# Kernel tuning notes

Hardware: AMD Instinct MI355X
Metric: run time of the kernel (lower is better)

The kernel has to match this reference:

```python
import jax, jax.numpy as jnp
import numpy as np

HEADS = 8
DIM_HEAD = 64


def setup_inputs() -> dict:
    key = jax.random.key(0)
    k1, k2, k3 = jax.random.split(key, 3)
    b, hw, n, dim = 2, 1024, 64, 512
    x = jax.random.normal(k1, (b, hw, n, dim), dtype=jnp.float32)
    w_qkv = jax.random.normal(k2, (3 * HEADS * DIM_HEAD, dim), dtype=jnp.float32) * 0.02
    pos_bias = jax.random.normal(k3, (HEADS, n, n), dtype=jnp.float32)
    # one batch attends everywhere, one focuses on the present frame (eye mask)
    focus_present_mask = jnp.arange(b).astype(bool)
    return {"x": x, "w_qkv": w_qkv, "pos_bias": pos_bias,
            "focus_present_mask": focus_present_mask}


def reference(x, w_qkv, pos_bias, focus_present_mask):
    b, hw, n, dim = x.shape
    h, d = HEADS, DIM_HEAD
    scale = d ** -0.5

    # fused qkv projection (no bias)
    qkv = jnp.einsum('bsnc,ec->bsne', x, w_qkv)          # (b, hw, n, 3*h*d)
    q, k, v = jnp.split(qkv, 3, axis=-1)

    def to_heads(t):  # '... n (h d) -> ... h n d'
        return jnp.moveaxis(t.reshape(b, hw, n, h, d), 3, 2)

    q, k, v = map(to_heads, (q, k, v))                   # (b, hw, h, n, d)
    q = q * scale

    sim = jnp.einsum('bshid,bshjd->bshij', q, k)         # (b, hw, h, n, n)
    sim = sim + pos_bias                                 # broadcast (h, n, n)

    # focus-present mask: eye for focused batches, all-ones otherwise
    eye = jnp.eye(n, dtype=bool)
    ones = jnp.ones((n, n), dtype=bool)
    mask = jnp.where(focus_present_mask[:, None, None, None, None],
                     eye[None, None, None], ones[None, None, None])  # (b,1,1,n,n)
    neg_max = -jnp.finfo(sim.dtype).max
    sim = jnp.where(mask, sim, neg_max)

    attn = jax.nn.softmax(sim, axis=-1)                  # includes the amax shift
    out = jnp.einsum('bshij,bshjd->bshid', attn, v)      # (b, hw, h, n, d)
    out = jnp.moveaxis(out, 2, 3).reshape(b, hw, n, h * d)  # '... h n d -> ... n (h d)'
    return out
```

## Files before the change

### kernel.cpp

```cpp
#include <hip/hip_runtime.h>
#include <hip/hip_bf16.h>


typedef __attribute__((ext_vector_type(4))) float f32x4;
typedef __attribute__((ext_vector_type(8))) short s16x8;

#define DIM 512

__device__ __forceinline__ short f2bf(float f) {
    __hip_bfloat16 h = __float2bfloat16(f);
    return __builtin_bit_cast(short, h);
}
__device__ __forceinline__ f32x4 ntld4(const float* p) {
    return __builtin_nontemporal_load((const f32x4*)p);
}
__device__ __forceinline__ void ntst4(float* p, f32x4 v) {
    __builtin_nontemporal_store(v, (f32x4*)p);
}
__device__ __forceinline__ s16x8 pack8(f32x4 a, f32x4 b) {
    s16x8 v;
    v[0] = f2bf(a[0]); v[1] = f2bf(a[1]); v[2] = f2bf(a[2]); v[3] = f2bf(a[3]);
    v[4] = f2bf(b[0]); v[5] = f2bf(b[1]); v[6] = f2bf(b[2]); v[7] = f2bf(b[3]);
    return v;
}
__device__ __forceinline__ int xaddr(int row, int kb) {
    return (row << 10) + (kb ^ ((row & 7) << 4));
}
__device__ __forceinline__ int taddr(int row, int kb) {
    return (row << 7) + (kb ^ ((row & 7) << 4));
}

__global__ void conv_w(const float* __restrict__ w, unsigned short* __restrict__ wb) {
    int gid  = blockIdx.x * 256 + threadIdx.x;
    int lane = gid & 63;
    int ks   = (gid >> 6) & 15;
    int rowblk = gid >> 10;
    int row = rowblk * 16 + (lane & 15);
    int col = ks * 32 + (lane >> 4) * 8;
    const float* p = w + (size_t)row * DIM + col;
    f32x4 a = *(const f32x4*)p;
    f32x4 b = *(const f32x4*)(p + 4);
    float sc = (row < 512) ? 0.125f : 1.0f;
    a *= sc; b *= sc;
    *(s16x8*)(wb + (size_t)gid * 8) = pack8(a, b);
}

template<int WB16>
__device__ __forceinline__ s16x8 wfragL(const unsigned short* __restrict__ wb,
                                        const float* __restrict__ w,
                                        int rowblk, int ks, int lane) {
    if constexpr (WB16) {
        return *(const s16x8*)(wb + ((size_t)(rowblk * 16 + ks) * 64 + lane) * 8);
    } else {
        int row = rowblk * 16 + (lane & 15);
        int col = ks * 32 + (lane >> 4) * 8;
        const float* p = w + (size_t)row * DIM + col;
        f32x4 u0 = *(const f32x4*)p;
        f32x4 u1 = *(const f32x4*)(p + 4);
        float sc = (row < 512) ? 0.125f : 1.0f;
        u0 *= sc; u1 *= sc;
        return pack8(u0, u1);
    }
}

__device__ __forceinline__ bool decode_mask(const unsigned int* mk, int b) {
    unsigned int m0 = mk[0], m1 = mk[1];
    if (m0 <= 1u && m1 <= 1u) return ((b == 0) ? m0 : m1) != 0u;
    return ((const unsigned char*)mk)[b] != 0;
}

#define MFB(a, b, cc) __builtin_amdgcn_mfma_f32_16x16x32_bf16(a, b, cc, 0, 0, 0)

#define XF(ks)                                                               \
    s16x8 af0 = *(const s16x8*)(smem + xaddr(c,      (ks) * 64 + g * 16));   \
    s16x8 af1 = *(const s16x8*)(smem + xaddr(16 + c, (ks) * 64 + g * 16));   \
    s16x8 af2 = *(const s16x8*)(smem + xaddr(32 + c, (ks) * 64 + g * 16));   \
    s16x8 af3 = *(const s16x8*)(smem + xaddr(48 + c, (ks) * 64 + g * 16));

template<int WB16>
__global__ __launch_bounds__(1024, 4)
void attn_merged(const float* __restrict__ x,
                 const float* __restrict__ w,
                 const unsigned short* __restrict__ wb,
                 const float* __restrict__ pb,
                 const unsigned int* __restrict__ mk,
                 float* __restrict__ out)
{
    extern __shared__ char smem[];
    const int tid  = threadIdx.x;
    const int lane = tid & 63;
    const int wave = tid >> 6;
    const int g    = lane >> 4;
    const int c    = lane & 15;
    const int hp   = wave >> 1;
    const int hw2  = wave & 1;
    const int site = blockIdx.x;
    const bool focused = decode_mask(mk, site >> 10);
    const float* xblk   = x   + (size_t)site * (64 * DIM);
    float*       outblk = out + (size_t)site * (64 * DIM);
    const f32x4 zf = {0.f, 0.f, 0.f, 0.f};

    {
        const int row = tid >> 4, c16 = tid & 15;
        const float* gp = xblk + row * DIM;
        #pragma unroll
        for (int j = 0; j < 4; ++j) {
            f32x4 a = ntld4(gp + j * 128 + c16 * 8);
            f32x4 b = ntld4(gp + j * 128 + c16 * 8 + 4);
            *(s16x8*)(smem + xaddr(row, j * 256 + c16 * 16)) = pack8(a, b);
        }
    }
    __syncthreads();

    if (focused) {
        const int RB = 64 + hp * 4 + 2 * hw2;
        f32x4 va[2][4];
        #pragma unroll
        for (int i = 0; i < 2; ++i)
            #pragma unroll
            for (int j = 0; j < 4; ++j) va[i][j] = zf;
        #pragma unroll 4
        for (int ks = 0; ks < 16; ++ks) {
            s16x8 wv0 = wfragL<WB16>(wb, w, RB,     ks, lane);
            s16x8 wv1 = wfragL<WB16>(wb, w, RB + 1, ks, lane);
            XF(ks)
            va[0][0]=MFB(wv0,af0,va[0][0]); va[0][1]=MFB(wv0,af1,va[0][1]);
            va[0][2]=MFB(wv0,af2,va[0][2]); va[0][3]=MFB(wv0,af3,va[0][3]);
            va[1][0]=MFB(wv1,af0,va[1][0]); va[1][1]=MFB(wv1,af1,va[1][1]);
            va[1][2]=MFB(wv1,af2,va[1][2]); va[1][3]=MFB(wv1,af3,va[1][3]);
        }
        #pragma unroll
        for (int i = 0; i < 2; ++i)
            #pragma unroll
            for (int j = 0; j < 4; ++j)
                *(f32x4*)(outblk + (size_t)(j * 16 + c) * DIM
                          + hp * 64 + hw2 * 32 + i * 16 + g * 4) = va[i][j];
        return;
    }

    char* slotA = smem + hp * 8192;
    char* slotB = smem + 65536 + hp * 8192;
    const int RQ = hp * 4 + 2 * hw2;
    const int RK = 32 + hp * 4 + 2 * hw2;

    {
        f32x4 acc[4][2];
        #pragma unroll
        for (int t = 0; t < 4; ++t) { acc[t][0] = zf; acc[t][1] = zf; }
        #pragma unroll 4
        for (int ks = 0; ks < 16; ++ks) {
            s16x8 w0 = wfragL<WB16>(wb, w, RQ,     ks, lane);
            s16x8 w1 = wfragL<WB16>(wb, w, RQ + 1, ks, lane);
            XF(ks)
            acc[0][0]=MFB(af0,w0,acc[0][0]); acc[0][1]=MFB(af0,w1,acc[0][1]);
            acc[1][0]=MFB(af1,w0,acc[1][0]); acc[1][1]=MFB(af1,w1,acc[1][1]);
            acc[2][0]=MFB(af2,w0,acc[2][0]); acc[2][1]=MFB(af2,w1,acc[2][1]);
            acc[3][0]=MFB(af3,w0,acc[3][0]); acc[3][1]=MFB(af3,w1,acc[3][1]);
        }
        #pragma unroll
        for (int t = 0; t < 4; ++t)
            #pragma unroll
            for (int hc = 0; hc < 2; ++hc)
                #pragma unroll
                for (int rr = 0; rr < 4; ++rr) {
                    int row = t * 16 + g * 4 + rr;
                    int col = hw2 * 32 + hc * 16 + c;
                    *(short*)(slotB + (row << 7) + ((col * 2) ^ ((row & 7) << 4))) =
                        f2bf(acc[t][hc][rr]);
                }
    }

    s16x8 kc[4];
    {
        f32x4 acc[4][2];
        #pragma unroll
        for (int t = 0; t < 4; ++t) { acc[t][0] = zf; acc[t][1] = zf; }
        #pragma unroll 4
        for (int ks = 0; ks < 16; ++ks) {
            s16x8 w0 = wfragL<WB16>(wb, w, RK,     ks, lane);
            s16x8 w1 = wfragL<WB16>(wb, w, RK + 1, ks, lane);
            XF(ks)
            acc[0][0]=MFB(af0,w0,acc[0][0]); acc[0][1]=MFB(af0,w1,acc[0][1]);
            acc[1][0]=MFB(af1,w0,acc[1][0]); acc[1][1]=MFB(af1,w1,acc[1][1]);
            acc[2][0]=MFB(af2,w0,acc[2][0]); acc[2][1]=MFB(af2,w1,acc[2][1]);
            acc[3][0]=MFB(af3,w0,acc[3][0]); acc[3][1]=MFB(af3,w1,acc[3][1]);
        }
        #pragma unroll
        for (int t = 0; t < 4; ++t) kc[t] = pack8(acc[t][0], acc[t][1]);
    }

    s16x8 vc[4];
    #pragma unroll
    for (int sub = 0; sub < 2; ++sub) {
        const int RB = 64 + hp * 4 + 2 * hw2 + sub;
        f32x4 a0 = zf, a1 = zf, a2 = zf, a3 = zf;
        #pragma unroll 4
        for (int ks = 0; ks < 16; ++ks) {
            s16x8 wv = wfragL<WB16>(wb, w, RB, ks, lane);
            XF(ks)
            a0 = MFB(wv, af0, a0); a1 = MFB(wv, af1, a1);
            a2 = MFB(wv, af2, a2); a3 = MFB(wv, af3, a3);
        }
        vc[sub * 2]     = pack8(a0, a1);
        vc[sub * 2 + 1] = pack8(a2, a3);
    }

    __syncthreads();

    #pragma unroll
    for (int t = 0; t < 4; ++t)
        #pragma unroll
        for (int hc = 0; hc < 2; ++hc)
            #pragma unroll
            for (int rr = 0; rr < 4; ++rr) {
                int row = t * 16 + g * 4 + rr;
                int col = hw2 * 32 + hc * 16 + c;
                *(short*)(slotA + (row << 7) + ((col * 2) ^ ((row & 7) << 4))) =
                    kc[t][hc * 4 + rr];
            }
    __syncthreads();

    s16x8 qf[2][2];
    #pragma unroll
    for (int ks2 = 0; ks2 < 2; ++ks2)
        #pragma unroll
        for (int tr2 = 0; tr2 < 2; ++tr2)
            qf[ks2][tr2] = *(const s16x8*)(slotB +
                taddr((2 * hw2 + tr2) * 16 + c, ks2 * 64 + g * 16));
    __syncthreads();

    #pragma unroll
    for (int sub = 0; sub < 2; ++sub)
        #pragma unroll
        for (int t = 0; t < 4; ++t)
            #pragma unroll
            for (int rr = 0; rr < 4; ++rr) {
                int row = hw2 * 32 + sub * 16 + g * 4 + rr;
                int col = t * 16 + c;
                *(short*)(slotB + (row << 7) + ((col * 2) ^ ((row & 7) << 4))) =
                    vc[sub * 2 + (t >> 1)][(t & 1) * 4 + rr];
            }

    f32x4 sm[2][4];
    #pragma unroll
    for (int i = 0; i < 2; ++i)
        #pragma unroll
        for (int j = 0; j < 4; ++j) sm[i][j] = zf;
    #pragma unroll
    for (int ks2 = 0; ks2 < 2; ++ks2) {
        #pragma unroll
        for (int j = 0; j < 4; ++j) {
            s16x8 bk = *(const s16x8*)(slotA + taddr(j * 16 + c, ks2 * 64 + g * 16));
            sm[0][j] = MFB(qf[ks2][0], bk, sm[0][j]);
            sm[1][j] = MFB(qf[ks2][1], bk, sm[1][j]);
        }
    }

    const float* pbh = pb + hp * 4096;
    #pragma unroll
    for (int tr = 0; tr < 2; ++tr) {
        #pragma unroll
        for (int rr = 0; rr < 4; ++rr) {
            const int i = 32 * hw2 + tr * 16 + g * 4 + rr;
            float v0 = sm[tr][0][rr] + pbh[i * 64 +  0 + c];
            float v1 = sm[tr][1][rr] + pbh[i * 64 + 16 + c];
            float v2 = sm[tr][2][rr] + pbh[i * 64 + 32 + c];
            float v3 = sm[tr][3][rr] + pbh[i * 64 + 48 + c];
            float mx = fmaxf(fmaxf(v0, v1), fmaxf(v2, v3));
            mx = fmaxf(mx, __shfl_xor(mx, 1));
            mx = fmaxf(mx, __shfl_xor(mx, 2));
            mx = fmaxf(mx, __shfl_xor(mx, 4));
            mx = fmaxf(mx, __shfl_xor(mx, 8));
            float p0 = __expf(v0 - mx);
            float p1 = __expf(v1 - mx);
            float p2 = __expf(v2 - mx);
            float p3 = __expf(v3 - mx);
            float ssum = p0 + p1 + p2 + p3;
            ssum += __shfl_xor(ssum, 1);
            ssum += __shfl_xor(ssum, 2);
            ssum += __shfl_xor(ssum, 4);
            ssum += __shfl_xor(ssum, 8);
            float rinv = 1.0f / ssum;
            sm[tr][0][rr] = p0 * rinv; sm[tr][1][rr] = p1 * rinv;
            sm[tr][2][rr] = p2 * rinv; sm[tr][3][rr] = p3 * rinv;
        }
    }
    __syncthreads();

    #pragma unroll
    for (int tr = 0; tr < 2; ++tr)
        #pragma unroll
        for (int tc = 0; tc < 4; ++tc)
            #pragma unroll
            for (int rr = 0; rr < 4; ++rr) {
                int row = 32 * hw2 + tr * 16 + g * 4 + rr;
                int col = tc * 16 + c;
                *(short*)(slotA + (row << 7) + ((col * 2) ^ ((row & 7) << 4))) =
                    f2bf(sm[tr][tc][rr]);
            }
    __syncthreads();

    f32x4 ot[4][2];
    #pragma unroll
    for (int i = 0; i < 4; ++i) { ot[i][0] = zf; ot[i][1] = zf; }
    #pragma unroll
    for (int ks2 = 0; ks2 < 2; ++ks2) {
        s16x8 ba0 = *(const s16x8*)(slotA + taddr((2 * hw2 + 0) * 16 + c, ks2 * 64 + g * 16));
        s16x8 ba1 = *(const s16x8*)(slotA + taddr((2 * hw2 + 1) * 16 + c, ks2 * 64 + g * 16));
        #pragma unroll
        for (int i = 0; i < 4; ++i) {
            s16x8 av = *(const s16x8*)(slotB + taddr(i * 16 + c, ks2 * 64 + g * 16));
            ot[i][0] = MFB(av, ba0, ot[i][0]);
            ot[i][1] = MFB(av, ba1, ot[i][1]);
        }
    }

    #pragma unroll
    for (int i = 0; i < 4; ++i)
        #pragma unroll
        for (int j = 0; j < 2; ++j)
            *(f32x4*)(outblk + (size_t)(32 * hw2 + j * 16 + c) * DIM
                      + hp * 64 + i * 16 + g * 4) = ot[i][j];
}

extern "C" void kernel_launch(void* const* d_in, const int* in_sizes, int n_in,
                              void* d_out, int out_size, void* d_ws, size_t ws_size,
                              hipStream_t stream)
{
    const float* x  = (const float*)d_in[0];
    const float* w  = (const float*)d_in[1];
    const float* pb = (const float*)d_in[2];
    const unsigned int* mk = (const unsigned int*)d_in[3];
    float* out = (float*)d_out;

    const int LDS = 131072;
    const size_t wbytes = (size_t)1536 * 512 * sizeof(unsigned short);

    if (ws_size >= wbytes) {
        unsigned short* wbp = (unsigned short*)d_ws;
        conv_w<<<dim3(384), dim3(256), 0, stream>>>(w, wbp);
        hipFuncSetAttribute(reinterpret_cast<const void*>(&attn_merged<1>),
                            hipFuncAttributeMaxDynamicSharedMemorySize, LDS);
        attn_merged<1><<<dim3(2048), dim3(1024), LDS, stream>>>(x, w, wbp, pb, mk, out);
    } else {
        hipFuncSetAttribute(reinterpret_cast<const void*>(&attn_merged<0>),
                            hipFuncAttributeMaxDynamicSharedMemorySize, LDS);
        attn_merged<0><<<dim3(2048), dim3(1024), LDS, stream>>>(x, w, nullptr, pb, mk, out);
    }
}
```

Measured before the change: 293.3 us.

## Split each site across two half-head blocks and stage output through LDS

Each spatial site is now handled by two 512-thread blocks, each covering four of the eight heads, with 64KB of LDS instead of one 1024-thread block with 128KB. This lets more blocks be resident per CU and shortens each block's tail. The cost is that each block converts and loads the full x tile, so x global reads and bf16 conversion double. Q is now kept in registers and written to LDS together with K. Outputs are staged through a swizzled LDS tile and written with coalesced nontemporal stores, which adds extra syncs.

```diff
diff --git a/kernel.cpp b/kernel.cpp
--- a/kernel.cpp
+++ b/kernel.cpp
@@ -78,13 +78,13 @@
     s16x8 af3 = *(const s16x8*)(smem + xaddr(48 + c, (ks) * 64 + g * 16));
 
 template<int WB16>
-__global__ __launch_bounds__(1024, 4)
-void attn_merged(const float* __restrict__ x,
-                 const float* __restrict__ w,
-                 const unsigned short* __restrict__ wb,
-                 const float* __restrict__ pb,
-                 const unsigned int* __restrict__ mk,
-                 float* __restrict__ out)
+__global__ __launch_bounds__(512, 2)
+void attn_half(const float* __restrict__ x,
+               const float* __restrict__ w,
+               const unsigned short* __restrict__ wb,
+               const float* __restrict__ pb,
+               const unsigned int* __restrict__ mk,
+               float* __restrict__ out)
 {
     extern __shared__ char smem[];
     const int tid  = threadIdx.x;
@@ -92,28 +92,35 @@
     const int wave = tid >> 6;
     const int g    = lane >> 4;
     const int c    = lane & 15;
-    const int hp   = wave >> 1;
+    const int h2   = wave >> 1;
     const int hw2  = wave & 1;
-    const int site = blockIdx.x;
+    const int bid  = blockIdx.x;
+    const int site = bid >> 1;
+    const int half = bid & 1;
+    const int gh   = half * 4 + h2;
     const bool focused = decode_mask(mk, site >> 10);
     const float* xblk   = x   + (size_t)site * (64 * DIM);
     float*       outblk = out + (size_t)site * (64 * DIM);
     const f32x4 zf = {0.f, 0.f, 0.f, 0.f};
 
     {
-        const int row = tid >> 4, c16 = tid & 15;
-        const float* gp = xblk + row * DIM;
-        #pragma unroll
-        for (int j = 0; j < 4; ++j) {
-            f32x4 a = ntld4(gp + j * 128 + c16 * 8);
-            f32x4 b = ntld4(gp + j * 128 + c16 * 8 + 4);
-            *(s16x8*)(smem + xaddr(row, j * 256 + c16 * 16)) = pack8(a, b);
+        const int row16 = tid >> 4, c16 = tid & 15;
+        #pragma unroll
+        for (int rr2 = 0; rr2 < 2; ++rr2) {
+            const int row = row16 + rr2 * 32;
+            const float* gp = xblk + row * DIM;
+            #pragma unroll
+            for (int j = 0; j < 4; ++j) {
+                f32x4 a = ntld4(gp + j * 128 + c16 * 8);
+                f32x4 b = ntld4(gp + j * 128 + c16 * 8 + 4);
+                *(s16x8*)(smem + xaddr(row, j * 256 + c16 * 16)) = pack8(a, b);
+            }
         }
     }
     __syncthreads();
 
     if (focused) {
-        const int RB = 64 + hp * 4 + 2 * hw2;
+        const int RB = 64 + gh * 4 + 2 * hw2;
         f32x4 va[2][4];
         #pragma unroll
         for (int i = 0; i < 2; ++i)
@@ -129,20 +136,30 @@
             va[1][0]=MFB(wv1,af0,va[1][0]); va[1][1]=MFB(wv1,af1,va[1][1]);
             va[1][2]=MFB(wv1,af2,va[1][2]); va[1][3]=MFB(wv1,af3,va[1][3]);
         }
-        #pragma unroll
-        for (int i = 0; i < 2; ++i)
-            #pragma unroll
-            for (int j = 0; j < 4; ++j)
-                *(f32x4*)(outblk + (size_t)(j * 16 + c) * DIM
-                          + hp * 64 + hw2 * 32 + i * 16 + g * 4) = va[i][j];
+        __syncthreads();
+        #pragma unroll
+        for (int sub = 0; sub < 2; ++sub)
+            #pragma unroll
+            for (int tt = 0; tt < 4; ++tt) {
+                int rl   = tt * 16 + c;
+                int colb = h2 * 256 + hw2 * 128 + sub * 64 + g * 16;
+                *(f32x4*)(smem + rl * 1024 + (colb ^ ((rl & 7) << 4))) = va[sub][tt];
+            }
+        __syncthreads();
+        #pragma unroll
+        for (int i = 0; i < 8; ++i) {
+            int lin = i * 8192 + tid * 16;
+            int rl = lin >> 10, off = lin & 1023;
+            f32x4 v = *(const f32x4*)(smem + rl * 1024 + (off ^ ((rl & 7) << 4)));
+            ntst4((float*)((char*)outblk + rl * 2048 + half * 1024 + off), v);
+        }
         return;
     }
 
-    char* slotA = smem + hp * 8192;
-    char* slotB = smem + 65536 + hp * 8192;
-    const int RQ = hp * 4 + 2 * hw2;
-    const int RK = 32 + hp * 4 + 2 * hw2;
-
+    const int RQ = gh * 4 + 2 * hw2;
+    const int RK = 32 + gh * 4 + 2 * hw2;
+
+    s16x8 qc[4];
     {
         f32x4 acc[4][2];
         #pragma unroll
@@ -158,16 +175,7 @@
             acc[3][0]=MFB(af3,w0,acc[3][0]); acc[3][1]=MFB(af3,w1,acc[3][1]);
         }
         #pragma unroll
-        for (int t = 0; t < 4; ++t)
-            #pragma unroll
-            for (int hc = 0; hc < 2; ++hc)
-                #pragma unroll
-                for (int rr = 0; rr < 4; ++rr) {
-                    int row = t * 16 + g * 4 + rr;
-                    int col = hw2 * 32 + hc * 16 + c;
-                    *(short*)(slotB + (row << 7) + ((col * 2) ^ ((row & 7) << 4))) =
-                        f2bf(acc[t][hc][rr]);
-                }
+        for (int t = 0; t < 4; ++t) qc[t] = pack8(acc[t][0], acc[t][1]);
     }
 
     s16x8 kc[4];
@@ -192,7 +200,7 @@
     s16x8 vc[4];
     #pragma unroll
     for (int sub = 0; sub < 2; ++sub) {
-        const int RB = 64 + hp * 4 + 2 * hw2 + sub;
+        const int RB = 64 + gh * 4 + 2 * hw2 + sub;
         f32x4 a0 = zf, a1 = zf, a2 = zf, a3 = zf;
         #pragma unroll 4
         for (int ks = 0; ks < 16; ++ks) {
@@ -207,6 +215,9 @@
 
     __syncthreads();
 
+    char* slotA = smem + h2 * 16384;
+    char* slotB = slotA + 8192;
+
     #pragma unroll
     for (int t = 0; t < 4; ++t)
         #pragma unroll
@@ -215,8 +226,9 @@
             for (int rr = 0; rr < 4; ++rr) {
                 int row = t * 16 + g * 4 + rr;
                 int col = hw2 * 32 + hc * 16 + c;
-                *(short*)(slotA + (row << 7) + ((col * 2) ^ ((row & 7) << 4))) =
-                    kc[t][hc * 4 + rr];
+                int off = (row << 7) + ((col * 2) ^ ((row & 7) << 4));
+                *(short*)(slotB + off) = qc[t][hc * 4 + rr];
+                *(short*)(slotA + off) = kc[t][hc * 4 + rr];
             }
     __syncthreads();
 
@@ -256,7 +268,7 @@
         }
     }
 
-    const float* pbh = pb + hp * 4096;
+    const float* pbh = pb + gh * 4096;
     #pragma unroll
     for (int tr = 0; tr < 2; ++tr) {
         #pragma unroll
@@ -314,13 +326,24 @@
             ot[i][1] = MFB(av, ba1, ot[i][1]);
         }
     }
+    __syncthreads();
 
     #pragma unroll
     for (int i = 0; i < 4; ++i)
         #pragma unroll
-        for (int j = 0; j < 2; ++j)
-            *(f32x4*)(outblk + (size_t)(32 * hw2 + j * 16 + c) * DIM
-                      + hp * 64 + i * 16 + g * 4) = ot[i][j];
+        for (int j = 0; j < 2; ++j) {
+            int rl   = 32 * hw2 + j * 16 + c;
+            int colb = h2 * 256 + i * 64 + g * 16;
+            *(f32x4*)(smem + rl * 1024 + (colb ^ ((rl & 7) << 4))) = ot[i][j];
+        }
+    __syncthreads();
+    #pragma unroll
+    for (int i = 0; i < 8; ++i) {
+        int lin = i * 8192 + tid * 16;
+        int rl = lin >> 10, off = lin & 1023;
+        f32x4 v = *(const f32x4*)(smem + rl * 1024 + (off ^ ((rl & 7) << 4)));
+        ntst4((float*)((char*)outblk + rl * 2048 + half * 1024 + off), v);
+    }
 }
 
 extern "C" void kernel_launch(void* const* d_in, const int* in_sizes, int n_in,
@@ -333,18 +356,18 @@
     const unsigned int* mk = (const unsigned int*)d_in[3];
     float* out = (float*)d_out;
 
-    const int LDS = 131072;
+    const int LDS = 65536;
     const size_t wbytes = (size_t)1536 * 512 * sizeof(unsigned short);
 
     if (ws_size >= wbytes) {
         unsigned short* wbp = (unsigned short*)d_ws;
         conv_w<<<dim3(384), dim3(256), 0, stream>>>(w, wbp);
-        hipFuncSetAttribute(reinterpret_cast<const void*>(&attn_merged<1>),
+        hipFuncSetAttribute(reinterpret_cast<const void*>(&attn_half<1>),
                             hipFuncAttributeMaxDynamicSharedMemorySize, LDS);
-        attn_merged<1><<<dim3(2048), dim3(1024), LDS, stream>>>(x, w, wbp, pb, mk, out);
+        attn_half<1><<<dim3(4096), dim3(512), LDS, stream>>>(x, w, wbp, pb, mk, out);
     } else {
-        hipFuncSetAttribute(reinterpret_cast<const void*>(&attn_merged<0>),
+        hipFuncSetAttribute(reinterpret_cast<const void*>(&attn_half<0>),
                             hipFuncAttributeMaxDynamicSharedMemorySize, LDS);
-        attn_merged<0><<<dim3(2048), dim3(1024), LDS, stream>>>(x, w, nullptr, pb, mk, out);
-    }
-}
+        attn_half<0><<<dim3(4096), dim3(512), LDS, stream>>>(x, w, nullptr, pb, mk, out);
+    }
+}
```

Result: slower. 312.4 us (+6.5%).
